# Kernel optimization log

Hardware: AMD Instinct MI355X
Metric: run time of the kernel (lower is better)

## Reference

```python
import jax, jax.numpy as jnp
import numpy as np

VOCAB, EMBED = 100000, 128
B, QLEN, DLEN = 1024, 32, 256
KERNEL_NUM, SIGMA, EXACT_SIGMA = 11, 0.1, 0.001
EPS = 1e-8  # torch F.cosine_similarity eps


def _kernel_mus(n):
    l_mu = [1.0]
    if n == 1:
        return l_mu
    bin_size = 2.0 / (n - 1)
    l_mu.append(1 - bin_size / 2)
    for i in range(1, n - 1):
        l_mu.append(round(l_mu[i] - bin_size, 5))
    return list(reversed(l_mu))


def _kernel_sigmas(n, sigma, exact_sigma):
    l_sigma = [exact_sigma]
    if n == 1:
        return l_sigma
    l_sigma += [sigma] * (n - 1)
    return list(reversed(l_sigma))


MUS = jnp.asarray(np.array(_kernel_mus(KERNEL_NUM), dtype=np.float32))      # [K]
SIGMAS = jnp.asarray(np.array(_kernel_sigmas(KERNEL_NUM, SIGMA, EXACT_SIGMA), dtype=np.float32))  # [K]


def setup_inputs() -> dict:
    key = jax.random.key(0)
    k = jax.random.split(key, 7)
    return {
        "emb": jax.random.normal(k[0], (VOCAB, EMBED), dtype=jnp.float32),
        "mlp_w": jax.random.normal(k[1], (1, KERNEL_NUM), dtype=jnp.float32) * 0.3,
        "mlp_b": jax.random.normal(k[2], (1,), dtype=jnp.float32) * 0.1,
        "query1": jax.random.randint(k[3], (B, QLEN), 0, VOCAB, dtype=jnp.int32).astype(jnp.int64),
        "doc1": jax.random.randint(k[4], (B, DLEN), 0, VOCAB, dtype=jnp.int32).astype(jnp.int64),
        "query2": jax.random.randint(k[5], (B, QLEN), 0, VOCAB, dtype=jnp.int32).astype(jnp.int64),
        "doc2": jax.random.randint(k[6], (B, DLEN), 0, VOCAB, dtype=jnp.int32).astype(jnp.int64),
    }


def _predict(emb, mlp_w, mlp_b, query, doc):
    qe = emb[query]                               # [B,Q,E]
    de = emb[doc]                                 # [B,D,E]
    qn = jnp.linalg.norm(qe, axis=-1)             # [B,Q]
    dn = jnp.linalg.norm(de, axis=-1)             # [B,D]
    dots = jnp.einsum("bqe,bde->bqd", qe, de)    # [B,Q,D]
    sim = dots / jnp.maximum(qn[:, :, None] * dn[:, None, :], EPS)
    # multi-Gaussian soft histogram: exp(-(sim-mu)^2/(2 sigma^2)), sum over doc,
    # log1p, sum over query  -> [B,K]
    z = (sim[..., None] - MUS) / SIGMAS           # [B,Q,D,K]
    K = jnp.exp(-0.5 * z * z)
    pooled = jnp.log1p(K.sum(axis=2)).sum(axis=1)  # [B,K]
    return pooled @ mlp_w.T + mlp_b               # [B,1]


def reference(emb, mlp_w, mlp_b, query1, doc1, query2, doc2):
    logits_1 = _predict(emb, mlp_w, mlp_b, query1, doc1)
    logits_2 = _predict(emb, mlp_w, mlp_b, query2, doc2)
    return jax.nn.sigmoid(logits_1 - logits_2)    # [B,1]
```

## Files before the change

### kernel.cpp

```cpp
#include <hip/hip_runtime.h>
#include <math.h>

#define VOCAB 100000
#define NB    1024
#define QLEN  32
#define DLEN  256
#define EMBED 128
#define KNUM  11

typedef __attribute__((ext_vector_type(8))) short bf16x8;
typedef __attribute__((ext_vector_type(4))) float f32x4;

#define HALF_L2E 0.7213475204444817f
#define TWO_L2E  2.8853900817779268f
#define EM4      0.018315638888734179f

#define SSTR  68
#define SHALF (16 * SSTR)

__global__ __launch_bounds__(256)
void cvt_table(const float* __restrict__ emb, ushort* __restrict__ ebf,
               float* __restrict__ inorm)
{
    const int row = blockIdx.x * 8 + (threadIdx.x >> 5);
    const int l32 = threadIdx.x & 31;
    const float4 v = *((const float4*)(emb + (size_t)row * EMBED) + l32);
    union { float f; unsigned u; } x0, x1, x2, x3;
    x0.f = v.x; x1.f = v.y; x2.f = v.z; x3.f = v.w;
    const unsigned r0 = x0.u + 0x8000u, r1 = x1.u + 0x8000u;
    const unsigned r2 = x2.u + 0x8000u, r3 = x3.u + 0x8000u;
    uint2 packed;
    packed.x = (r0 >> 16) | (r1 & 0xFFFF0000u);
    packed.y = (r2 >> 16) | (r3 & 0xFFFF0000u);
    *((uint2*)(ebf + (size_t)row * EMBED) + l32) = packed;
    x0.u = r0 & 0xFFFF0000u; x1.u = r1 & 0xFFFF0000u;
    x2.u = r2 & 0xFFFF0000u; x3.u = r3 & 0xFFFF0000u;
    float n = x0.f * x0.f + x1.f * x1.f + x2.f * x2.f + x3.f * x3.f;
    #pragma unroll
    for (int m = 1; m < 32; m <<= 1) n += __shfl_xor(n, m);
    if (l32 == 0) inorm[row] = __builtin_amdgcn_rsqf(n);
}

__device__ __forceinline__ bf16x8 cvt8(const float* p, float& nacc)
{
    uint4 a = *((const uint4*)p);
    uint4 b = *((const uint4*)(p + 4));
    unsigned u[8] = {a.x, a.y, a.z, a.w, b.x, b.y, b.z, b.w};
    bf16x8 r;
    #pragma unroll
    for (int i = 0; i < 8; ++i) {
        const unsigned q = u[i] + 0x8000u;
        r[i] = (short)(q >> 16);
        union { unsigned uu; float ff; } g; g.uu = q & 0xFFFF0000u;
        nacc = fmaf(g.ff, g.ff, nacc);
    }
    return r;
}

__device__ __forceinline__ void pool_half(float* __restrict__ wtile,
                                          const f32x4* __restrict__ a,
                                          const float* __restrict__ riq,
                                          const float* __restrict__ idn,
                                          float (*__restrict__ stot)[12],
                                          int mtbase, int l15, int quad)
{
    #pragma unroll
    for (int nt = 0; nt < 4; ++nt)
        #pragma unroll
        for (int r = 0; r < 4; ++r)
            wtile[(quad * 4 + r) * SSTR + nt * 16 + l15] = a[nt][r] * riq[r] * idn[nt];

    const float* rp = wtile + l15 * SSTR + quad * 16;
    float ksum[KNUM];
    #pragma unroll
    for (int k = 0; k < KNUM; ++k) ksum[k] = 0.f;

    #pragma unroll
    for (int i = 0; i < 4; ++i) {
        const f32x4 sv = *((const f32x4*)(rp + 4 * i));
        #pragma unroll
        for (int e = 0; e < 4; ++e) {
            const float s  = sv[e];
            const float z  = fmaf(s, 10.f, -1.f);
            const float e0 = exp2f(-HALF_L2E * (z * z));
            float ru = exp2f(fmaf(z,  TWO_L2E, -TWO_L2E));
            float rd = exp2f(fmaf(z, -TWO_L2E, -TWO_L2E));
            ksum[5] += e0;
            float tt = e0;
            tt *= ru; ksum[6] += tt; ru *= EM4;
            tt *= ru; ksum[7] += tt; ru *= EM4;
            tt *= ru; ksum[8] += tt; ru *= EM4;
            tt *= ru; ksum[9] += tt;
            tt = e0;
            tt *= rd; ksum[4] += tt; rd *= EM4;
            tt *= rd; ksum[3] += tt; rd *= EM4;
            tt *= rd; ksum[2] += tt; rd *= EM4;
            tt *= rd; ksum[1] += tt; rd *= EM4;
            tt *= rd; ksum[0] += tt;
            ksum[10] += (s > 0.995f) ? 1.f : 0.f;
        }
    }
    #pragma unroll
    for (int k = 0; k < KNUM; ++k) {
        ksum[k] += __shfl_xor(ksum[k], 16);
        ksum[k] += __shfl_xor(ksum[k], 32);
    }
    if (quad == 0) {
        #pragma unroll
        for (int k = 0; k < KNUM; ++k)
            atomicAdd(&stot[mtbase + l15][k], ksum[k]);
    }
}

template<bool PRE>
__global__ __launch_bounds__(256, 4)
void knrm_pair(const float* __restrict__ emb,
               const ushort* __restrict__ ebf,
               const float* __restrict__ inorm,
               const float* __restrict__ mlp_w,
               const int* __restrict__ q1, const int* __restrict__ d1,
               const int* __restrict__ q2, const int* __restrict__ d2,
               float* __restrict__ logits)
{
    const int b    = blockIdx.x;
    const int pair = blockIdx.y;
    const int t    = threadIdx.x;
    const int w    = t >> 6;
    const int l15  = t & 15;
    const int quad = (t & 63) >> 4;

    const int* __restrict__ qry = (pair == 0 ? q1 : q2) + b * QLEN;
    const int* __restrict__ doc = (pair == 0 ? d1 : d2) + b * DLEN;

    __shared__ __align__(16) float s_sim[4 * SHALF];
    __shared__ float s_tot[QLEN][12];

    #pragma unroll
    for (int i = t; i < QLEN * 12; i += 256) ((float*)s_tot)[i] = 0.f;
    __syncthreads();

    const int qid0 = qry[l15], qid1 = qry[l15 + 16];
    int did[4];
    #pragma unroll
    for (int nt = 0; nt < 4; ++nt) did[nt] = doc[(w * 4 + nt) * 16 + l15];

    f32x4 acc[2][4];
    #pragma unroll
    for (int mt = 0; mt < 2; ++mt)
        #pragma unroll
        for (int nt = 0; nt < 4; ++nt)
            acc[mt][nt] = (f32x4){0.f, 0.f, 0.f, 0.f};

    float idn[4], riq[2][4];
    float* wtile = s_sim + w * SHALF;

    if (PRE) {
        const ushort* qp0 = ebf + (size_t)qid0 * EMBED + quad * 8;
        const ushort* qp1 = ebf + (size_t)qid1 * EMBED + quad * 8;
        #pragma unroll
        for (int kk = 0; kk < 4; ++kk) {
            const bf16x8 a0 = *((const bf16x8*)(qp0 + kk * 32));
            const bf16x8 a1 = *((const bf16x8*)(qp1 + kk * 32));
            #pragma unroll
            for (int nt = 0; nt < 4; ++nt) {
                const bf16x8 bb = *((const bf16x8*)(ebf + (size_t)did[nt] * EMBED + quad * 8 + kk * 32));
                acc[0][nt] = __builtin_amdgcn_mfma_f32_16x16x32_bf16(a0, bb, acc[0][nt], 0, 0, 0);
                acc[1][nt] = __builtin_amdgcn_mfma_f32_16x16x32_bf16(a1, bb, acc[1][nt], 0, 0, 0);
            }
        }
        #pragma unroll
        for (int nt = 0; nt < 4; ++nt) idn[nt] = inorm[did[nt]];
        #pragma unroll
        for (int r = 0; r < 4; ++r) {
            riq[0][r] = inorm[qry[quad * 4 + r]];
            riq[1][r] = inorm[qry[16 + quad * 4 + r]];
        }
    } else {
        float qn2[2] = {0.f, 0.f}, dn2[4] = {0.f, 0.f, 0.f, 0.f};
        const float* qp0 = emb + (size_t)qid0 * EMBED + quad * 8;
        const float* qp1 = emb + (size_t)qid1 * EMBED + quad * 8;
        #pragma unroll
        for (int kk = 0; kk < 4; ++kk) {
            const bf16x8 a0 = cvt8(qp0 + kk * 32, qn2[0]);
            const bf16x8 a1 = cvt8(qp1 + kk * 32, qn2[1]);
            #pragma unroll
            for (int nt = 0; nt < 4; ++nt) {
                const bf16x8 bb = cvt8(emb + (size_t)did[nt] * EMBED + quad * 8 + kk * 32, dn2[nt]);
                acc[0][nt] = __builtin_amdgcn_mfma_f32_16x16x32_bf16(a0, bb, acc[0][nt], 0, 0, 0);
                acc[1][nt] = __builtin_amdgcn_mfma_f32_16x16x32_bf16(a1, bb, acc[1][nt], 0, 0, 0);
            }
        }
        #pragma unroll
        for (int i = 0; i < 2; ++i) {
            qn2[i] += __shfl_xor(qn2[i], 16);
            qn2[i] += __shfl_xor(qn2[i], 32);
        }
        #pragma unroll
        for (int nt = 0; nt < 4; ++nt) {
            dn2[nt] += __shfl_xor(dn2[nt], 16);
            dn2[nt] += __shfl_xor(dn2[nt], 32);
            idn[nt] = __builtin_amdgcn_rsqf(dn2[nt]);
        }
        #pragma unroll
        for (int r = 0; r < 4; ++r) {
            riq[0][r] = __builtin_amdgcn_rsqf(__shfl(qn2[0], quad * 4 + r));
            riq[1][r] = __builtin_amdgcn_rsqf(__shfl(qn2[1], quad * 4 + r));
        }
    }

    pool_half(wtile, acc[0], riq[0], idn, s_tot, 0,  l15, quad);
    pool_half(wtile, acc[1], riq[1], idn, s_tot, 16, l15, quad);
    __syncthreads();

    if (t < QLEN) {
        float c = 0.f;
        #pragma unroll
        for (int k = 0; k < KNUM; ++k) c += mlp_w[k] * log1pf(s_tot[t][k]);
        #pragma unroll
        for (int mm = 1; mm < 32; mm <<= 1) c += __shfl_xor(c, mm);
        if (t == 0) logits[pair * NB + b] = c;
    }
}

__global__ __launch_bounds__(256)
void knrm_combine(const float* __restrict__ logits, float* __restrict__ out)
{
    const int i = blockIdx.x * blockDim.x + threadIdx.x;
    if (i < NB) {
        const float d = logits[i] - logits[NB + i];
        out[i] = 1.f / (1.f + __expf(-d));
    }
}

extern "C" void kernel_launch(void* const* d_in, const int* in_sizes, int n_in,
                              void* d_out, int out_size, void* d_ws, size_t ws_size,
                              hipStream_t stream)
{
    const float* emb   = (const float*)d_in[0];
    const float* mlp_w = (const float*)d_in[1];
    const int* q1 = (const int*)d_in[3];
    const int* d1 = (const int*)d_in[4];
    const int* q2 = (const int*)d_in[5];
    const int* d2 = (const int*)d_in[6];

    float* out = (float*)d_out;

    const size_t need = 2 * NB * 4
                      + (size_t)VOCAB * 4
                      + (size_t)VOCAB * EMBED * 2 + 256;
    dim3 grid(NB, 2);
    if (ws_size >= need) {
        float*  logits = (float*)d_ws;
        float*  inorm  = logits + 2 * NB;
        ushort* ebf    = (ushort*)(inorm + VOCAB);
        cvt_table<<<VOCAB / 8, 256, 0, stream>>>(emb, ebf, inorm);
        knrm_pair<true><<<grid, 256, 0, stream>>>(emb, ebf, inorm, mlp_w,
                                                  q1, d1, q2, d2, logits);
    } else {
        float* logits = (float*)d_ws;
        knrm_pair<false><<<grid, 256, 0, stream>>>(emb, nullptr, nullptr, mlp_w,
                                                   q1, d1, q2, d2, logits);
    }
    knrm_combine<<<(NB + 255) / 256, 256, 0, stream>>>((float*)d_ws, out);
}
```

Before: 145.5 us.

## Add streaming knrm_pair2 kernel with async global-to-LDS doc prefetch pipeline

Replaces the fast-path pair kernel with a new 128-thread kernel. Each wave keeps its 16 query rows in registers, and doc embedding chunks are streamed through a 4-deep LDS ring using global_load_lds with explicit vmcnt waits. Each 16-column tile goes through MFMA and is pooled into the Gaussian kernel sums right away, instead of computing full tiles first and accumulating them with atomics. This is meant to overlap gather latency with compute and cut LDS traffic and atomics, at the cost of a barrier per tile and a smaller block.

```diff
diff --git a/kernel.cpp b/kernel.cpp
--- a/kernel.cpp
+++ b/kernel.cpp
@@ -1,5 +1,6 @@
 #include <hip/hip_runtime.h>
 #include <math.h>
+#include <stdint.h>
 
 #define VOCAB 100000
 #define NB    1024
@@ -41,43 +42,115 @@
     if (l32 == 0) inorm[row] = __builtin_amdgcn_rsqf(n);
 }
 
-__device__ __forceinline__ bf16x8 cvt8(const float* p, float& nacc)
-{
-    uint4 a = *((const uint4*)p);
-    uint4 b = *((const uint4*)(p + 4));
-    unsigned u[8] = {a.x, a.y, a.z, a.w, b.x, b.y, b.z, b.w};
-    bf16x8 r;
-    #pragma unroll
-    for (int i = 0; i < 8; ++i) {
-        const unsigned q = u[i] + 0x8000u;
-        r[i] = (short)(q >> 16);
-        union { unsigned uu; float ff; } g; g.uu = q & 0xFFFF0000u;
-        nacc = fmaf(g.ff, g.ff, nacc);
-    }
-    return r;
-}
-
-__device__ __forceinline__ void pool_half(float* __restrict__ wtile,
-                                          const f32x4* __restrict__ a,
-                                          const float* __restrict__ riq,
-                                          const float* __restrict__ idn,
-                                          float (*__restrict__ stot)[12],
-                                          int mtbase, int l15, int quad)
-{
-    #pragma unroll
-    for (int nt = 0; nt < 4; ++nt)
+__device__ __forceinline__ void gl_lds16(const ushort* g, ushort* lds)
+{
+    auto gp = reinterpret_cast<const __attribute__((address_space(1))) void*>(
+        reinterpret_cast<uintptr_t>(g));
+    auto lp = reinterpret_cast<__attribute__((address_space(3))) void*>(
+        static_cast<unsigned>(reinterpret_cast<uintptr_t>(lds)));
+    __builtin_amdgcn_global_load_lds(gp, lp, 16, 0, 0);
+}
+
+#define WAITV(n) asm volatile("s_waitcnt vmcnt(" #n ")" ::: "memory")
+
+__global__ __launch_bounds__(128, 4)
+void knrm_pair2(const ushort* __restrict__ ebf,
+                const float* __restrict__ inorm,
+                const float* __restrict__ mlp_w,
+                const int* __restrict__ q1, const int* __restrict__ d1,
+                const int* __restrict__ q2, const int* __restrict__ d2,
+                float* __restrict__ logits)
+{
+    const int b    = blockIdx.x;
+    const int pair = blockIdx.y;
+    const int t    = threadIdx.x;
+    const int w    = t >> 6;
+    const int l    = t & 63;
+    const int l15  = l & 15;
+    const int quad = l >> 4;
+
+    const int* __restrict__ qry = (pair == 0 ? q1 : q2) + b * QLEN;
+    const int* __restrict__ doc = (pair == 0 ? d1 : d2) + b * DLEN;
+
+    __shared__ __align__(16) ushort s_doc[4][4][64][8];
+    __shared__ __align__(16) float  s_sim[2][16][20];
+    __shared__ float s_part[2];
+
+    int dcid[16];
+    #pragma unroll
+    for (int c = 0; c < 16; ++c) dcid[c] = doc[c * 16 + l15];
+    const int qid = qry[w * 16 + l15];
+    int qrr[4];
+    #pragma unroll
+    for (int r = 0; r < 4; ++r) qrr[r] = qry[w * 16 + quad * 4 + r];
+
+    float idnv[16];
+    #pragma unroll
+    for (int c = 0; c < 16; ++c) idnv[c] = inorm[dcid[c]];
+    float riqw[4];
+    #pragma unroll
+    for (int r = 0; r < 4; ++r) riqw[r] = inorm[qrr[r]];
+    bf16x8 aq[4];
+    {
+        const ushort* qp = ebf + (size_t)qid * EMBED + quad * 8;
+        #pragma unroll
+        for (int kk = 0; kk < 4; ++kk) aq[kk] = *(const bf16x8*)(qp + kk * 32);
+    }
+    float wk[KNUM];
+    #pragma unroll
+    for (int k = 0; k < KNUM; ++k) wk[k] = mlp_w[k];
+
+    #define STAGE(c)                                                              \
+    {                                                                             \
+        const ushort* gbase = ebf + (size_t)dcid[c] * EMBED + quad * 8;           \
+        gl_lds16(gbase + (2 * w) * 32,     &s_doc[(c) & 3][2 * w][0][0]);         \
+        gl_lds16(gbase + (2 * w + 1) * 32, &s_doc[(c) & 3][2 * w + 1][0][0]);     \
+    }
+
+    STAGE(0); STAGE(1); STAGE(2);
+
+    float ksum[KNUM];
+    #pragma unroll
+    for (int k = 0; k < KNUM; ++k) ksum[k] = 0.f;
+
+    #pragma unroll
+    for (int nt = 0; nt < 16; ++nt) {
+        if      (nt <= 13) WAITV(4);
+        else if (nt == 14) WAITV(2);
+        else               WAITV(0);
+        __builtin_amdgcn_s_barrier();
+        __builtin_amdgcn_sched_barrier(0);
+
+        if (nt + 3 < 16) {
+            switch (nt + 3) {
+                case 3:  STAGE(3);  break;
+                case 4:  STAGE(4);  break;
+                case 5:  STAGE(5);  break;
+                case 6:  STAGE(6);  break;
+                case 7:  STAGE(7);  break;
+                case 8:  STAGE(8);  break;
+                case 9:  STAGE(9);  break;
+                case 10: STAGE(10); break;
+                case 11: STAGE(11); break;
+                case 12: STAGE(12); break;
+                case 13: STAGE(13); break;
+                case 14: STAGE(14); break;
+                case 15: STAGE(15); break;
+            }
+        }
+
+        f32x4 acc = {0.f, 0.f, 0.f, 0.f};
+        #pragma unroll
+        for (int kk = 0; kk < 4; ++kk) {
+            const bf16x8 bb = *(const bf16x8*)&s_doc[nt & 3][kk][l][0];
+            acc = __builtin_amdgcn_mfma_f32_16x16x32_bf16(aq[kk], bb, acc, 0, 0, 0);
+        }
+
+        const float idn_c = idnv[nt];
         #pragma unroll
         for (int r = 0; r < 4; ++r)
-            wtile[(quad * 4 + r) * SSTR + nt * 16 + l15] = a[nt][r] * riq[r] * idn[nt];
-
-    const float* rp = wtile + l15 * SSTR + quad * 16;
-    float ksum[KNUM];
-    #pragma unroll
-    for (int k = 0; k < KNUM; ++k) ksum[k] = 0.f;
-
-    #pragma unroll
-    for (int i = 0; i < 4; ++i) {
-        const f32x4 sv = *((const f32x4*)(rp + 4 * i));
+            s_sim[w][quad * 4 + r][l15] = acc[r] * riqw[r] * idn_c;
+        const f32x4 sv = *(const f32x4*)&s_sim[w][l15][quad * 4];
         #pragma unroll
         for (int e = 0; e < 4; ++e) {
             const float s  = sv[e];
@@ -100,6 +173,82 @@
             ksum[10] += (s > 0.995f) ? 1.f : 0.f;
         }
     }
+    #undef STAGE
+
+    #pragma unroll
+    for (int k = 0; k < KNUM; ++k) {
+        ksum[k] += __shfl_xor(ksum[k], 16);
+        ksum[k] += __shfl_xor(ksum[k], 32);
+    }
+    float c = 0.f;
+    #pragma unroll
+    for (int k = 0; k < KNUM; ++k) c += wk[k] * log1pf(ksum[k]);
+    c += __shfl_xor(c, 1); c += __shfl_xor(c, 2);
+    c += __shfl_xor(c, 4); c += __shfl_xor(c, 8);
+    if (l == 0) s_part[w] = c;
+    __syncthreads();
+    if (t == 0) logits[pair * NB + b] = s_part[0] + s_part[1];
+}
+
+__device__ __forceinline__ bf16x8 cvt8(const float* p, float& nacc)
+{
+    uint4 a = *((const uint4*)p);
+    uint4 b = *((const uint4*)(p + 4));
+    unsigned u[8] = {a.x, a.y, a.z, a.w, b.x, b.y, b.z, b.w};
+    bf16x8 r;
+    #pragma unroll
+    for (int i = 0; i < 8; ++i) {
+        const unsigned q = u[i] + 0x8000u;
+        r[i] = (short)(q >> 16);
+        union { unsigned uu; float ff; } g; g.uu = q & 0xFFFF0000u;
+        nacc = fmaf(g.ff, g.ff, nacc);
+    }
+    return r;
+}
+
+__device__ __forceinline__ void pool_half(float* __restrict__ wtile,
+                                          const f32x4* __restrict__ a,
+                                          const float* __restrict__ riq,
+                                          const float* __restrict__ idn,
+                                          float (*__restrict__ stot)[12],
+                                          int mtbase, int l15, int quad)
+{
+    #pragma unroll
+    for (int nt = 0; nt < 4; ++nt)
+        #pragma unroll
+        for (int r = 0; r < 4; ++r)
+            wtile[(quad * 4 + r) * SSTR + nt * 16 + l15] = a[nt][r] * riq[r] * idn[nt];
+
+    const float* rp = wtile + l15 * SSTR + quad * 16;
+    float ksum[KNUM];
+    #pragma unroll
+    for (int k = 0; k < KNUM; ++k) ksum[k] = 0.f;
+
+    #pragma unroll
+    for (int i = 0; i < 4; ++i) {
+        const f32x4 sv = *((const f32x4*)(rp + 4 * i));
+        #pragma unroll
+        for (int e = 0; e < 4; ++e) {
+            const float s  = sv[e];
+            const float z  = fmaf(s, 10.f, -1.f);
+            const float e0 = exp2f(-HALF_L2E * (z * z));
+            float ru = exp2f(fmaf(z,  TWO_L2E, -TWO_L2E));
+            float rd = exp2f(fmaf(z, -TWO_L2E, -TWO_L2E));
+            ksum[5] += e0;
+            float tt = e0;
+            tt *= ru; ksum[6] += tt; ru *= EM4;
+            tt *= ru; ksum[7] += tt; ru *= EM4;
+            tt *= ru; ksum[8] += tt; ru *= EM4;
+            tt *= ru; ksum[9] += tt;
+            tt = e0;
+            tt *= rd; ksum[4] += tt; rd *= EM4;
+            tt *= rd; ksum[3] += tt; rd *= EM4;
+            tt *= rd; ksum[2] += tt; rd *= EM4;
+            tt *= rd; ksum[1] += tt; rd *= EM4;
+            tt *= rd; ksum[0] += tt;
+            ksum[10] += (s > 0.995f) ? 1.f : 0.f;
+        }
+    }
     #pragma unroll
     for (int k = 0; k < KNUM; ++k) {
         ksum[k] += __shfl_xor(ksum[k], 16);
@@ -248,18 +397,17 @@
     const size_t need = 2 * NB * 4
                       + (size_t)VOCAB * 4
                       + (size_t)VOCAB * EMBED * 2 + 256;
-    dim3 grid(NB, 2);
     if (ws_size >= need) {
         float*  logits = (float*)d_ws;
         float*  inorm  = logits + 2 * NB;
         ushort* ebf    = (ushort*)(inorm + VOCAB);
         cvt_table<<<VOCAB / 8, 256, 0, stream>>>(emb, ebf, inorm);
-        knrm_pair<true><<<grid, 256, 0, stream>>>(emb, ebf, inorm, mlp_w,
-                                                  q1, d1, q2, d2, logits);
+        knrm_pair2<<<dim3(NB, 2), 128, 0, stream>>>(ebf, inorm, mlp_w,
+                                                    q1, d1, q2, d2, logits);
     } else {
         float* logits = (float*)d_ws;
-        knrm_pair<false><<<grid, 256, 0, stream>>>(emb, nullptr, nullptr, mlp_w,
-                                                   q1, d1, q2, d2, logits);
+        knrm_pair<false><<<dim3(NB, 2), 256, 0, stream>>>(emb, nullptr, nullptr, mlp_w,
+                                                          q1, d1, q2, d2, logits);
     }
     knrm_combine<<<(NB + 255) / 256, 256, 0, stream>>>((float*)d_ws, out);
 }
```

New measurement: 187.3 us. +28.7%, slower.
